# Kernel tuning notes

Hardware: AMD Instinct MI355X
Metric: run time of the kernel (lower is better)

The kernel has to match this reference:

```python
import jax, jax.numpy as jnp
import numpy as np

N = 100000
E = 1600000
F_IN = 512
H1, C1 = 8, 8      # layer-1: 8 heads, 8 dims each (concat -> 64)
H2, C2 = 1, 16     # layer-2: 1 head, num_classes=16
SLOPE = 0.2        # GATConv leaky_relu negative slope


def setup_inputs() -> dict:
    key = jax.random.key(0)
    ks = jax.random.split(key, 10)
    x = jax.random.normal(ks[0], (N, F_IN), dtype=jnp.float32)
    edge_index = jax.random.randint(ks[1], (2, E), 0, N, dtype=jnp.int32)
    s = 0.05
    W1 = jax.random.normal(ks[2], (F_IN, H1 * C1), dtype=jnp.float32) * s
    a1_src = jax.random.normal(ks[3], (H1, C1), dtype=jnp.float32) * s
    a1_dst = jax.random.normal(ks[4], (H1, C1), dtype=jnp.float32) * s
    b1 = jnp.zeros((H1 * C1,), dtype=jnp.float32)
    W2 = jax.random.normal(ks[5], (H1 * C1, H2 * C2), dtype=jnp.float32) * s
    a2_src = jax.random.normal(ks[6], (H2, C2), dtype=jnp.float32) * s
    a2_dst = jax.random.normal(ks[7], (H2, C2), dtype=jnp.float32) * s
    b2 = jnp.zeros((H2 * C2,), dtype=jnp.float32)
    return {"x": x, "edge_index": edge_index, "W1": W1, "a1_src": a1_src,
            "a1_dst": a1_dst, "b1": b1, "W2": W2, "a2_src": a2_src,
            "a2_dst": a2_dst, "b2": b2}


def _gat_conv(h, src, dst, W, a_src, a_dst, b, heads, ch):
    n = h.shape[0]
    hp = (h @ W).reshape(n, heads, ch)                      # [N,H,C]
    al_s = jnp.einsum('nhc,hc->nh', hp, a_src)              # [N,H]
    al_d = jnp.einsum('nhc,hc->nh', hp, a_dst)              # [N,H]
    e = jax.nn.leaky_relu(al_s[src] + al_d[dst], SLOPE)     # [E,H]
    # segment softmax over edges sharing a destination (self-loops guarantee >=1 edge/node)
    emax = jax.lax.stop_gradient(jax.ops.segment_max(e, dst, num_segments=n))
    ee = jnp.exp(e - emax[dst])
    denom = jax.ops.segment_sum(ee, dst, num_segments=n)
    alpha = ee / denom[dst]                                 # [E,H]
    msg = hp[src] * alpha[:, :, None]                       # [E,H,C]
    out = jax.ops.segment_sum(msg, dst, num_segments=n)     # [N,H,C]
    return out.reshape(n, heads * ch) + b


def reference(x, edge_index, W1, a1_src, a1_dst, b1, W2, a2_src, a2_dst, b2):
    n = x.shape[0]
    loops = jnp.arange(n, dtype=edge_index.dtype)           # add_self_loops=True
    src = jnp.concatenate([edge_index[0], loops])
    dst = jnp.concatenate([edge_index[1], loops])
    h = jax.nn.elu(_gat_conv(x, src, dst, W1, a1_src, a1_dst, b1, H1, C1))
    h = _gat_conv(h, src, dst, W2, a2_src, a2_dst, b2, H2, C2)
    return jax.nn.log_softmax(h, axis=1)
```

## Files before the change

kernel.cpp:

```cpp
#include <hip/hip_runtime.h>
#include <hip/hip_bf16.h>

#define N_NODES 100000
#define F_IN    512
#define H1      8
#define C1      8
#define D1      64
#define C2      16
#define SLOPE   0.2f
#define CAP     48
#define PSHIFT  9
#define PPART   196
#define CAPP    9216
#define CHUNK   4096

typedef __bf16 bf16_t;
typedef bf16_t bf16x8 __attribute__((ext_vector_type(8)));
typedef float  f32x4  __attribute__((ext_vector_type(4)));

__global__ __launch_bounds__(256) void part_kernel(
    const float* __restrict__ W1, bf16_t* __restrict__ W1b,
    const int* __restrict__ ei, int* __restrict__ pcnt, int2* __restrict__ pfifo,
    int E, int total)
{
    __shared__ int hist[PPART];
    __shared__ int lofs[PPART];
    __shared__ int gbase[PPART];
    __shared__ int cursor[PPART];
    __shared__ int sdata[256];
    __shared__ int2 fifo[CHUNK];

    const int t = threadIdx.x;
    const int chunk0 = (int)blockIdx.x * CHUNK;

    for (int i = (int)blockIdx.x * 256 + t; i < 64 * 512; i += (int)gridDim.x * 256) {
        int nn = i >> 9, k = i & 511;
        W1b[i] = (bf16_t)W1[k * 64 + nn];
    }

    for (int i = t; i < PPART; i += 256) hist[i] = 0;
    __syncthreads();

    int srcs[16], dsts[16];
    const int e0 = chunk0 + t * 16;
    if (e0 + 16 <= E) {
#pragma unroll
        for (int q = 0; q < 4; ++q) {
            int4 s = *(const int4*)(ei + e0 + q * 4);
            int4 d = *(const int4*)(ei + E + e0 + q * 4);
            srcs[q*4+0]=s.x; srcs[q*4+1]=s.y; srcs[q*4+2]=s.z; srcs[q*4+3]=s.w;
            dsts[q*4+0]=d.x; dsts[q*4+1]=d.y; dsts[q*4+2]=d.z; dsts[q*4+3]=d.w;
        }
    } else {
#pragma unroll
        for (int j = 0; j < 16; ++j) {
            int e = e0 + j;
            if (e < E)          { srcs[j] = ei[e]; dsts[j] = ei[E + e]; }
            else if (e < total) { srcs[j] = dsts[j] = e - E; }
            else                { srcs[j] = -1;    dsts[j] = -1; }
        }
    }
#pragma unroll
    for (int j = 0; j < 16; ++j)
        if (dsts[j] >= 0) atomicAdd(&hist[dsts[j] >> PSHIFT], 1);
    __syncthreads();

    int hv = (t < PPART) ? hist[t] : 0;
    sdata[t] = hv;
    __syncthreads();
    for (int off = 1; off < 256; off <<= 1) {
        int x = (t >= off) ? sdata[t - off] : 0;
        __syncthreads();
        sdata[t] += x;
        __syncthreads();
    }
    if (t < PPART) {
        int lo = sdata[t] - hv;
        lofs[t]   = lo;
        cursor[t] = lo;
        gbase[t]  = hv ? atomicAdd(&pcnt[t], hv) : 0;
    }
    __syncthreads();

#pragma unroll
    for (int j = 0; j < 16; ++j) {
        if (dsts[j] >= 0) {
            int p = dsts[j] >> PSHIFT;
            int slot = atomicAdd(&cursor[p], 1);
            fifo[slot] = make_int2(srcs[j], dsts[j]);
        }
    }
    __syncthreads();

    const int w = t >> 6, lane = t & 63;
    for (int p = w; p < PPART; p += 4) {
        int len = hist[p];
        int lo  = lofs[p];
        int gb  = gbase[p];
        int2* dstp = pfifo + (size_t)p * CAPP;
        for (int j = lane; j < len; j += 64) {
            int g = gb + j;
            if (g < CAPP) dstp[g] = fifo[lo + j];
        }
    }
}

__global__ __launch_bounds__(512, 4) void pg_kernel(
    const int2* __restrict__ pfifo, const int* __restrict__ pcnt,
    int* __restrict__ buckets, int* __restrict__ cnt,
    const float* __restrict__ X, const bf16_t* __restrict__ Bt,
    const float* __restrict__ a1s, const float* __restrict__ a1d,
    bf16_t* __restrict__ HPb, float* __restrict__ als1, float* __restrict__ ald1,
    int n)
{
    __shared__ int lcnt[1 << PSHIFT];
    __shared__ __align__(16) bf16_t Bsm[8 * 4 * 64 * 8];

    const int t = threadIdx.x;

    if (blockIdx.x < PPART) {
        const int p = blockIdx.x;
        const int dbase = p << PSHIFT;
        const int nd = min(1 << PSHIFT, n - dbase);
        for (int i = t; i < nd; i += 512) lcnt[i] = 0;
        __syncthreads();

        int len = pcnt[p]; if (len > CAPP) len = CAPP;
        const int2* f = pfifo + (size_t)p * CAPP;

        int i = t;
        for (; i + 1536 < len; i += 2048) {
            int2 e0 = f[i], e1 = f[i + 512], e2 = f[i + 1024], e3 = f[i + 1536];
            int s0 = atomicAdd(&lcnt[e0.y - dbase], 1);
            int s1 = atomicAdd(&lcnt[e1.y - dbase], 1);
            int s2 = atomicAdd(&lcnt[e2.y - dbase], 1);
            int s3 = atomicAdd(&lcnt[e3.y - dbase], 1);
            if (s0 < CAP) buckets[(size_t)e0.y * CAP + s0] = e0.x;
            if (s1 < CAP) buckets[(size_t)e1.y * CAP + s1] = e1.x;
            if (s2 < CAP) buckets[(size_t)e2.y * CAP + s2] = e2.x;
            if (s3 < CAP) buckets[(size_t)e3.y * CAP + s3] = e3.x;
        }
        for (; i < len; i += 512) {
            int2 e = f[i];
            int s = atomicAdd(&lcnt[e.y - dbase], 1);
            if (s < CAP) buckets[(size_t)e.y * CAP + s] = e.x;
        }
        __syncthreads();
        for (int i2 = t; i2 < nd; i2 += 512) cnt[dbase + i2] = min(lcnt[i2], CAP);
        return;
    }

    const int rowbase = ((int)blockIdx.x - PPART) * 128;
    const int w = t >> 6;
    const int lane = t & 63;

    const int rloc = lane & 15;
    const int koff = (lane >> 4) * 8;

    int grow = rowbase + w * 16 + rloc;
    int growc = (grow < n) ? grow : (n - 1);
    const float* arow = X + (size_t)growc * F_IN + koff;

    f32x4 acc[4];
#pragma unroll
    for (int nt = 0; nt < 4; ++nt) acc[nt] = (f32x4){0.f, 0.f, 0.f, 0.f};

#pragma unroll
    for (int half = 0; half < 2; ++half) {
        for (int i = t; i < 2048; i += 512) {
            int l9 = i & 63;
            int nt = (i >> 6) & 3;
            int ks = i >> 8;
            int row = nt * 16 + (l9 & 15);
            int col = (half * 8 + ks) * 32 + (l9 >> 4) * 8;
            *(bf16x8*)(Bsm + (size_t)i * 8) =
                *(const bf16x8*)(Bt + (size_t)row * F_IN + col);
        }
        __syncthreads();

#pragma unroll 4
        for (int ks = 0; ks < 8; ++ks) {
            int kg = (half * 8 + ks) * 32;
            float4 xa0 = *(const float4*)(arow + kg);
            float4 xa1 = *(const float4*)(arow + kg + 4);
            bf16x8 af;
            af[0]=(bf16_t)xa0.x; af[1]=(bf16_t)xa0.y; af[2]=(bf16_t)xa0.z; af[3]=(bf16_t)xa0.w;
            af[4]=(bf16_t)xa1.x; af[5]=(bf16_t)xa1.y; af[6]=(bf16_t)xa1.z; af[7]=(bf16_t)xa1.w;
#pragma unroll
            for (int nt = 0; nt < 4; ++nt) {
                bf16x8 b = *(const bf16x8*)(Bsm + ((ks * 4 + nt) * 64 + lane) * 8);
                acc[nt] = __builtin_amdgcn_mfma_f32_16x16x32_bf16(af, b, acc[nt], 0, 0, 0);
            }
        }
        __syncthreads();
    }

    const int colg = lane & 15;
    const int quad = lane >> 4;
    const int b    = colg >> 3;
    float cs[4], cd[4];
#pragma unroll
    for (int nt = 0; nt < 4; ++nt) {
        cs[nt] = a1s[nt * 16 + colg];
        cd[nt] = a1d[nt * 16 + colg];
    }

#pragma unroll
    for (int i = 0; i < 4; ++i) {
        int r = rowbase + w * 16 + quad * 4 + i;
        bool ok = r < n;
        if (ok) {
            bf16_t* hr = HPb + (size_t)r * D1;
            hr[colg]      = (bf16_t)acc[0][i];
            hr[16 + colg] = (bf16_t)acc[1][i];
            hr[32 + colg] = (bf16_t)acc[2][i];
            hr[48 + colg] = (bf16_t)acc[3][i];
        }
#pragma unroll
        for (int nt = 0; nt < 4; ++nt) {
            float ps = acc[nt][i] * cs[nt];
            float pd = acc[nt][i] * cd[nt];
            ps += __shfl_xor(ps, 1, 64);  pd += __shfl_xor(pd, 1, 64);
            ps += __shfl_xor(ps, 2, 64);  pd += __shfl_xor(pd, 2, 64);
            ps += __shfl_xor(ps, 4, 64);  pd += __shfl_xor(pd, 4, 64);
            if (ok && (colg & 7) == 0) {
                als1[(size_t)r * 8 + 2 * nt + b] = ps;
                ald1[(size_t)r * 8 + 2 * nt + b] = pd;
            }
        }
    }
}

#define AGG1_SEC(G0)                                                        \
    {                                                                       \
        float a_[16], v_[16];                                               \
        _Pragma("unroll")                                                   \
        for (int j = 0; j < 16; ++j) {                                      \
            int s = (G0 + j < m) ? idx[G0 + j] : 0;                         \
            a_[j] = als[s * 8 + h];                                         \
            v_[j] = (float)hp1[(size_t)s * D1 + lane];                      \
        }                                                                   \
        _Pragma("unroll")                                                   \
        for (int j = 0; j < 16; ++j) {                                      \
            float e = a_[j] + ad;                                           \
            e = (e > 0.f) ? e : SLOPE * e;                                  \
            float wgt = __expf(e);                                          \
            if (G0 + j >= m) wgt = 0.f;                                     \
            den += wgt;                                                     \
            acc = fmaf(wgt, v_[j], acc);                                    \
        }                                                                   \
    }

__global__ __launch_bounds__(256, 2) void agg1_kernel(
    const bf16_t* __restrict__ hp1,
    const float* __restrict__ als, const float* __restrict__ ald,
    const int* __restrict__ cnt, const int* __restrict__ buckets,
    const float* __restrict__ b1,
    const float* __restrict__ W2,
    const float* __restrict__ a2s, const float* __restrict__ a2d,
    bf16_t* __restrict__ HP2b, float* __restrict__ als2, float* __restrict__ ald2,
    int n)
{
    __shared__ float Wsm[64 * 17];
    const int t = threadIdx.x;
    for (int i = t; i < 1024; i += 256)
        Wsm[(i >> 4) * 17 + (i & 15)] = W2[i];
    __syncthreads();

    int node = blockIdx.x * 4 + (t >> 6);
    if (node >= n) return;
    int lane = t & 63;
    int h = lane >> 3;

    int m = cnt[node]; if (m > CAP) m = CAP;
    const int* bp = buckets + (size_t)node * CAP;
    float ad = ald[node * 8 + h];

    int idx[48];
#pragma unroll
    for (int q = 0; q < 12; ++q) {
        int4 v4 = *(const int4*)(bp + q * 4);
        idx[q*4+0] = v4.x; idx[q*4+1] = v4.y; idx[q*4+2] = v4.z; idx[q*4+3] = v4.w;
    }

    float den = 0.f, acc = 0.f;
    AGG1_SEC(0);
    if (m > 16) AGG1_SEC(16);
    if (m > 32) AGG1_SEC(32);

    float v = acc / den + b1[lane];
    v = (v > 0.f) ? v : (__expf(v) - 1.f);

    const int g2 = lane >> 4, c = lane & 15;
    float o = 0.f;
#pragma unroll
    for (int kk = 0; kk < 16; ++kk) {
        float hk = __shfl(v, g2 * 16 + kk, 64);
        o = fmaf(hk, Wsm[(g2 * 16 + kk) * 17 + c], o);
    }
    o += __shfl_xor(o, 16, 64);
    o += __shfl_xor(o, 32, 64);
    if (g2 == 0) HP2b[(size_t)node * 16 + c] = (bf16_t)o;

    float rs = o * a2s[c];
    float rd = o * a2d[c];
    rs += __shfl_xor(rs, 1, 64);  rd += __shfl_xor(rd, 1, 64);
    rs += __shfl_xor(rs, 2, 64);  rd += __shfl_xor(rd, 2, 64);
    rs += __shfl_xor(rs, 4, 64);  rd += __shfl_xor(rd, 4, 64);
    rs += __shfl_xor(rs, 8, 64);  rd += __shfl_xor(rd, 8, 64);
    if (lane == 0) { als2[node] = rs; ald2[node] = rd; }
}

#define AGG2_SEC(G0)                                                        \
    {                                                                       \
        float a_[16], v_[16];                                               \
        _Pragma("unroll")                                                   \
        for (int j = 0; j < 16; ++j) {                                      \
            int s = (G0 + j < m) ? idx[G0 + j] : 0;                         \
            a_[j] = als[s];                                                 \
            v_[j] = (float)hp2[(size_t)s * 16 + c];                         \
        }                                                                   \
        _Pragma("unroll")                                                   \
        for (int j = 0; j < 16; ++j) {                                      \
            float e = a_[j] + ad;                                           \
            e = (e > 0.f) ? e : SLOPE * e;                                  \
            float wgt = __expf(e);                                          \
            if (G0 + j >= m) wgt = 0.f;                                     \
            den += wgt;                                                     \
            acc = fmaf(wgt, v_[j], acc);                                    \
        }                                                                   \
    }

__global__ __launch_bounds__(256, 2) void agg2_kernel(
    const bf16_t* __restrict__ hp2,
    const float* __restrict__ als, const float* __restrict__ ald,
    const int* __restrict__ cnt, const int* __restrict__ buckets,
    const float* __restrict__ b2,
    float* __restrict__ out, int n)
{
    int node = blockIdx.x * 16 + (threadIdx.x >> 4);
    if (node >= n) return;
    int c = threadIdx.x & 15;

    int m = cnt[node]; if (m > CAP) m = CAP;
    const int* bp = buckets + (size_t)node * CAP;
    float ad = ald[node];

    int idx[48];
#pragma unroll
    for (int q = 0; q < 12; ++q) {
        int4 v4 = *(const int4*)(bp + q * 4);
        idx[q*4+0] = v4.x; idx[q*4+1] = v4.y; idx[q*4+2] = v4.z; idx[q*4+3] = v4.w;
    }

    float den = 0.f, acc = 0.f;
    AGG2_SEC(0);
    if (m > 16) AGG2_SEC(16);
    if (m > 32) AGG2_SEC(32);

    float v = acc / den + b2[c];

    float mx = v;
    mx = fmaxf(mx, __shfl_xor(mx, 8, 16));
    mx = fmaxf(mx, __shfl_xor(mx, 4, 16));
    mx = fmaxf(mx, __shfl_xor(mx, 2, 16));
    mx = fmaxf(mx, __shfl_xor(mx, 1, 16));
    float ex = __expf(v - mx);
    float sum = ex;
    sum += __shfl_xor(sum, 8, 16);
    sum += __shfl_xor(sum, 4, 16);
    sum += __shfl_xor(sum, 2, 16);
    sum += __shfl_xor(sum, 1, 16);
    out[(size_t)node * 16 + c] = v - mx - __logf(sum);
}

extern "C" void kernel_launch(void* const* d_in, const int* in_sizes, int n_in,
                              void* d_out, int out_size, void* d_ws, size_t ws_size,
                              hipStream_t stream)
{
    const float* x      = (const float*)d_in[0];
    const int*   ei     = (const int*)  d_in[1];
    const float* W1     = (const float*)d_in[2];
    const float* a1_src = (const float*)d_in[3];
    const float* a1_dst = (const float*)d_in[4];
    const float* b1     = (const float*)d_in[5];
    const float* W2     = (const float*)d_in[6];
    const float* a2_src = (const float*)d_in[7];
    const float* a2_dst = (const float*)d_in[8];
    const float* b2     = (const float*)d_in[9];
    float* out = (float*)d_out;

    const int N = in_sizes[0] / F_IN;
    const int E = in_sizes[1] / 2;
    const int TOT = E + N;

    char* base = (char*)d_ws;
    size_t off = 0;
    auto carve = [&](size_t bytes) -> char* {
        char* p = base + off;
        off += (bytes + 255) & ~(size_t)255;
        return p;
    };
    bf16_t* hp1b    = (bf16_t*)carve((size_t)N * D1 * 2);
    float*  h1      = (float*) carve((size_t)N * D1 * 4);
    bf16_t* hp2b    = (bf16_t*)carve((size_t)N * 16 * 2);
    float*  als1    = (float*) carve((size_t)N * 8 * 4);
    float*  ald1    = (float*) carve((size_t)N * 8 * 4);
    float*  als2    = (float*) carve((size_t)N * 4);
    float*  ald2    = (float*) carve((size_t)N * 4);
    int*    cnt     = (int*)   carve((size_t)N * 4);
    int*    pcnt    = (int*)   carve((size_t)PPART * 4);
    int*    buckets = (int*)   carve((size_t)N * CAP * 4);
    bf16_t* W1b     = (bf16_t*)carve((size_t)64 * 512 * 2);
    int2*  pfifo   = (int2*)h1;

    const int Gp = (TOT + CHUNK - 1) / CHUNK;
    const int Gg = (N + 127) / 128;

    hipMemsetAsync(pcnt, 0, (size_t)PPART * 4, stream);

    part_kernel<<<Gp, 256, 0, stream>>>(W1, W1b, ei, pcnt, pfifo, E, TOT);

    pg_kernel<<<PPART + Gg, 512, 0, stream>>>(pfifo, pcnt, buckets, cnt,
                                              x, W1b, a1_src, a1_dst,
                                              hp1b, als1, ald1, N);

    agg1_kernel<<<(N + 3) / 4, 256, 0, stream>>>(hp1b, als1, ald1, cnt, buckets,
                                                 b1, W2, a2_src, a2_dst,
                                                 hp2b, als2, ald2, N);

    agg2_kernel<<<(N + 15) / 16, 256, 0, stream>>>(hp2b, als2, ald2, cnt, buckets, b2, out, N);
}
```

Measured before the change: 516.5 us.

## Precompute per-edge attention weights once into LDS in both aggregation kernels

Instead of each of the 8 lanes per head redundantly computing leaky_relu and exp for every neighbor, lanes now split neighbors, compute each edge weight once, store it in shared memory and reduce the denominator with shuffles. The gather loop then reads weights from LDS and neighbor indices straight from the bucket array instead of a 48-entry register array, which lowers register pressure. No barrier is placed between the LDS writes and the reads. That relies on each node's work staying inside one wavefront, and adds LDS traffic per edge.

```diff
diff --git a/kernel.cpp b/kernel.cpp
--- a/kernel.cpp
+++ b/kernel.cpp
@@ -233,21 +233,13 @@
 
 #define AGG1_SEC(G0)                                                        \
     {                                                                       \
-        float a_[16], v_[16];                                               \
         _Pragma("unroll")                                                   \
-        for (int j = 0; j < 16; ++j) {                                      \
-            int s = (G0 + j < m) ? idx[G0 + j] : 0;                         \
-            a_[j] = als[s * 8 + h];                                         \
-            v_[j] = (float)hp1[(size_t)s * D1 + lane];                      \
-        }                                                                   \
-        _Pragma("unroll")                                                   \
-        for (int j = 0; j < 16; ++j) {                                      \
-            float e = a_[j] + ad;                                           \
-            e = (e > 0.f) ? e : SLOPE * e;                                  \
-            float wgt = __expf(e);                                          \
-            if (G0 + j >= m) wgt = 0.f;                                     \
-            den += wgt;                                                     \
-            acc = fmaf(wgt, v_[j], acc);                                    \
+        for (int j = G0; j < G0 + 16; ++j) {                                \
+            int s = bp[j];                                                  \
+            s = (j < m) ? s : 0;           \
+            float wgt = wbuf[wv][h][j];                                     \
+            float v = (float)hp1[(size_t)s * D1 + lane];                    \
+            acc = fmaf(wgt, v, acc);                                        \
         }                                                                   \
     }
 
@@ -262,28 +254,43 @@
     int n)
 {
     __shared__ float Wsm[64 * 17];
+    __shared__ float wbuf[4][8][50];
+
     const int t = threadIdx.x;
     for (int i = t; i < 1024; i += 256)
         Wsm[(i >> 4) * 17 + (i & 15)] = W2[i];
     __syncthreads();
 
-    int node = blockIdx.x * 4 + (t >> 6);
+    const int wv = t >> 6;
+    const int lane = t & 63;
+    int node = blockIdx.x * 4 + wv;
     if (node >= n) return;
-    int lane = t & 63;
-    int h = lane >> 3;
+    node = __builtin_amdgcn_readfirstlane(node);
+    const int h = lane >> 3;
 
     int m = cnt[node]; if (m > CAP) m = CAP;
+    m = __builtin_amdgcn_readfirstlane(m);
     const int* bp = buckets + (size_t)node * CAP;
     float ad = ald[node * 8 + h];
 
-    int idx[48];
-#pragma unroll
-    for (int q = 0; q < 12; ++q) {
-        int4 v4 = *(const int4*)(bp + q * 4);
-        idx[q*4+0] = v4.x; idx[q*4+1] = v4.y; idx[q*4+2] = v4.z; idx[q*4+3] = v4.w;
-    }
-
-    float den = 0.f, acc = 0.f;
+    const int jbase = lane & 7;
+    float wsum = 0.f;
+#pragma unroll
+    for (int r = 0; r < 6; ++r) {
+        int j = jbase + 8 * r;
+        int s = (j < m) ? bp[j] : 0;
+        float e = als[s * 8 + h] + ad;
+        e = (e > 0.f) ? e : SLOPE * e;
+        float wgt = (j < m) ? __expf(e) : 0.f;
+        wbuf[wv][h][j] = wgt;
+        wsum += wgt;
+    }
+    wsum += __shfl_xor(wsum, 1, 64);
+    wsum += __shfl_xor(wsum, 2, 64);
+    wsum += __shfl_xor(wsum, 4, 64);
+    const float den = wsum;
+
+    float acc = 0.f;
     AGG1_SEC(0);
     if (m > 16) AGG1_SEC(16);
     if (m > 32) AGG1_SEC(32);
@@ -313,21 +320,13 @@
 
 #define AGG2_SEC(G0)                                                        \
     {                                                                       \
-        float a_[16], v_[16];                                               \
         _Pragma("unroll")                                                   \
-        for (int j = 0; j < 16; ++j) {                                      \
-            int s = (G0 + j < m) ? idx[G0 + j] : 0;                         \
-            a_[j] = als[s];                                                 \
-            v_[j] = (float)hp2[(size_t)s * 16 + c];                         \
-        }                                                                   \
-        _Pragma("unroll")                                                   \
-        for (int j = 0; j < 16; ++j) {                                      \
-            float e = a_[j] + ad;                                           \
-            e = (e > 0.f) ? e : SLOPE * e;                                  \
-            float wgt = __expf(e);                                          \
-            if (G0 + j >= m) wgt = 0.f;                                     \
-            den += wgt;                                                     \
-            acc = fmaf(wgt, v_[j], acc);                                    \
+        for (int j = G0; j < G0 + 16; ++j) {                                \
+            int s = bp[j];                                                  \
+            s = (j < m) ? s : 0;                                            \
+            float wgt = wbuf[nib][j];                                       \
+            float v = (float)hp2[(size_t)s * 16 + c];                       \
+            acc = fmaf(wgt, v, acc);                                        \
         }                                                                   \
     }
 
@@ -338,22 +337,35 @@
     const float* __restrict__ b2,
     float* __restrict__ out, int n)
 {
-    int node = blockIdx.x * 16 + (threadIdx.x >> 4);
+    __shared__ float wbuf[16][50];
+    const int t = threadIdx.x;
+    const int nib = t >> 4;
+    int node = blockIdx.x * 16 + nib;
     if (node >= n) return;
-    int c = threadIdx.x & 15;
+    const int c = t & 15;
 
     int m = cnt[node]; if (m > CAP) m = CAP;
     const int* bp = buckets + (size_t)node * CAP;
     float ad = ald[node];
 
-    int idx[48];
-#pragma unroll
-    for (int q = 0; q < 12; ++q) {
-        int4 v4 = *(const int4*)(bp + q * 4);
-        idx[q*4+0] = v4.x; idx[q*4+1] = v4.y; idx[q*4+2] = v4.z; idx[q*4+3] = v4.w;
-    }
-
-    float den = 0.f, acc = 0.f;
+    float wsum = 0.f;
+#pragma unroll
+    for (int r = 0; r < 3; ++r) {
+        int j = c + 16 * r;
+        int s = (j < m) ? bp[j] : 0;
+        float e = als[s] + ad;
+        e = (e > 0.f) ? e : SLOPE * e;
+        float wgt = (j < m) ? __expf(e) : 0.f;
+        wbuf[nib][j] = wgt;
+        wsum += wgt;
+    }
+    wsum += __shfl_xor(wsum, 1, 16);
+    wsum += __shfl_xor(wsum, 2, 16);
+    wsum += __shfl_xor(wsum, 4, 16);
+    wsum += __shfl_xor(wsum, 8, 16);
+    const float den = wsum;
+
+    float acc = 0.f;
     AGG2_SEC(0);
     if (m > 16) AGG2_SEC(16);
     if (m > 32) AGG2_SEC(32);
```

After: 468.2 us. 1.1x faster.
